# Performance work log

Measured on AMD Instinct MI355X. Metric: run time of the kernel, lower is better.

The kernel has to match this reference:

```python
import jax, jax.numpy as jnp
import numpy as np

N, H, W, C_SH = 512, 256, 256, 16
FX = FY = 300.0


def setup_inputs() -> dict:
    key = jax.random.key(0)
    ks = jax.random.split(key, 6)
    xy = jax.random.uniform(ks[0], (N, 2), minval=-0.8, maxval=0.8)
    z = jax.random.uniform(ks[1], (N, 1), minval=2.0, maxval=6.0)
    xyz = jnp.concatenate([xy * z, z], axis=-1).astype(jnp.float32)  # in frustum
    opacity = jax.random.uniform(ks[2], (N, 1), minval=0.1, maxval=1.0)
    features = jax.random.normal(ks[3], (N, C_SH, 3), dtype=jnp.float32) * 0.3
    A = jax.random.normal(ks[4], (N, 3, 3), dtype=jnp.float32) * 0.05
    covariance = jnp.einsum('nij,nkj->nik', A, A) + 1e-6 * jnp.eye(3, dtype=jnp.float32)
    K = jnp.array([[FX, 0.0, W / 2], [0.0, FY, H / 2], [0.0, 0.0, 1.0]], dtype=jnp.float32)
    w2c = jnp.eye(4, dtype=jnp.float32)
    bg = jnp.zeros(3, jnp.float32)
    return {"xyz": xyz, "opacity": opacity, "features": features,
            "covariance": covariance, "K": K, "w2c": w2c, "bg": bg}


def sh_to_rgb(sh, vd):
    # sh: (N,16,3), vd: (N,3) unit view dirs; degree-3 real SH basis
    C0, C1 = 0.28209479177387814, 0.4886025119029199
    x, y, z = vd[:, 0:1], vd[:, 1:2], vd[:, 2:3]
    r = sh[:, 0] * C0
    r = r + C1 * (-y * sh[:, 1] + z * sh[:, 2] - x * sh[:, 3])
    xx, yy, zz = x * x, y * y, z * z
    xy, yz, xz = x * y, y * z, x * z
    r = r + (1.0925484305920792 * xy * sh[:, 4]
             - 1.0925484305920792 * yz * sh[:, 5]
             + 0.31539156525252005 * (2.0 * zz - xx - yy) * sh[:, 6]
             - 1.0925484305920792 * xz * sh[:, 7]
             + 0.5462742152960396 * (xx - yy) * sh[:, 8])
    r = r + (-0.5900435899266435 * y * (3.0 * xx - yy) * sh[:, 9]
             + 2.890611442640554 * xy * z * sh[:, 10]
             - 0.4570457994644658 * y * (4.0 * zz - xx - yy) * sh[:, 11]
             + 0.3731763325901154 * z * (2.0 * zz - 3.0 * xx - 3.0 * yy) * sh[:, 12]
             - 0.4570457994644658 * x * (4.0 * zz - xx - yy) * sh[:, 13]
             + 1.445305721320277 * z * (xx - yy) * sh[:, 14]
             - 0.5900435899266435 * x * (xx - 3.0 * yy) * sh[:, 15])
    return jnp.clip(r + 0.5, 0.0, 1.0)


def render_gaussians(xyz, opacity, features, covariance, K, w2c, bg):
    R, t = w2c[:3, :3], w2c[:3, 3]
    xyz_cam = xyz @ R.T + t                      # (N,3)
    depth = xyz_cam[:, 2]
    xy_h = xyz_cam @ K.T
    xy = xy_h[:, :2] / jnp.clip(xy_h[:, 2:3], 1e-8)
    cam_pos = jnp.linalg.inv(w2c)[:3, 3]
    vd = xyz - cam_pos
    vd = vd / jnp.clip(jnp.linalg.norm(vd, axis=-1, keepdims=True), 1e-12)
    rgb = sh_to_rgb(features, vd)                # (N,3)

    # 2D covariance via perspective Jacobian: Sigma2d = (J W S W^T J^T)[:2,:2] + 0.3 I
    tz = jnp.clip(xyz_cam[:, 2], 1e-8)
    tx, ty = xyz_cam[:, 0], xyz_cam[:, 1]
    fx, fy = K[0, 0], K[1, 1]
    zr = jnp.zeros_like(tz)
    tz2 = tz * tz
    J = jnp.stack([fx / tz, zr, -fx * tx / tz2,
                   zr, fy / tz, -fy * ty / tz2,
                   zr, zr, zr], axis=-1).reshape(-1, 3, 3)
    T = jnp.einsum('nij,jk->nik', J, R)
    cov_cam = jnp.einsum('nij,njk,nlk->nil', T, covariance, T)
    cov2d = cov_cam[:, :2, :2] + 0.3 * jnp.eye(2, dtype=xyz.dtype)

    margin = 256.0
    visible = ((depth > 0.01) & (xy[:, 0] > -margin) & (xy[:, 0] < W + margin)
               & (xy[:, 1] > -margin) & (xy[:, 1] < H + margin))

    a, b, d = cov2d[:, 0, 0], cov2d[:, 0, 1], cov2d[:, 1, 1]
    det = a * d - b * b
    trace = a + d
    lam_max = 0.5 * (trace + jnp.sqrt(jnp.clip(trace * trace - 4.0 * det, 0.0)))
    radii_f = 3.0 * jnp.sqrt(jnp.clip(lam_max, 1e-8))
    radii = jnp.where(visible, radii_f, 0.0)
    det_c = jnp.clip(det, 1e-10)
    inv00, inv01, inv11 = d / det_c, -b / det_c, a / det_c

    # depth sort (invisible pushed to back; they contribute zero alpha)
    order = jnp.argsort(jnp.where(visible, depth, jnp.inf))
    mx, my = xy[order, 0], xy[order, 1]
    dep, op, col = depth[order], opacity[order, 0], rgb[order]
    i00, i01, i11 = inv00[order], inv01[order], inv11[order]
    rad = jnp.clip(radii_f[order], 1.0)
    vis = visible[order]

    gx = jnp.arange(W, dtype=xyz.dtype)
    gy = jnp.arange(H, dtype=xyz.dtype)
    dx = gx[None, None, :] - mx[:, None, None]   # (N,1,W) -> bcast (N,H,W)
    dy = gy[None, :, None] - my[:, None, None]
    maha = (i00[:, None, None] * dx * dx
            + 2.0 * i01[:, None, None] * dx * dy
            + i11[:, None, None] * dy * dy)
    weight = jnp.exp(-0.5 * maha)

    # per-gaussian screen box (mirrors the int()-floored crop in the torch loop)
    xlo = jnp.floor(jnp.clip(mx - rad, 0.0, W))
    xhi = jnp.floor(jnp.clip(mx + rad + 1.0, 0.0, W))
    ylo = jnp.floor(jnp.clip(my - rad, 0.0, H))
    yhi = jnp.floor(jnp.clip(my + rad + 1.0, 0.0, H))
    inbox = ((gx[None, None, :] >= xlo[:, None, None]) & (gx[None, None, :] < xhi[:, None, None])
             & (gy[None, :, None] >= ylo[:, None, None]) & (gy[None, :, None] < yhi[:, None, None]))

    alpha = jnp.clip(op[:, None, None] * weight, 0.0, 0.99)
    alpha = jnp.where(inbox & vis[:, None, None], alpha, 0.0)   # (N,H,W)

    # front-to-back alpha compositing via exclusive cumprod in log space
    log1m = jnp.log1p(-alpha)
    logT_excl = jnp.cumsum(log1m, axis=0) - log1m
    Tn = jnp.exp(logT_excl)
    wgt = Tn * alpha                                            # (N,H,W)
    T_final = jnp.exp(logT_excl[-1] + log1m[-1])                # (H,W)

    render = jnp.einsum('nhw,nc->chw', wgt, col) + bg[:, None, None] * T_final
    depth_img = jnp.sum(wgt * dep[:, None, None], axis=0)[None]
    alpha_img = (1.0 - T_final)[None]
    return render, depth_img, alpha_img, radii


def reference(xyz, opacity, features, covariance, K, w2c, bg):
    return render_gaussians(xyz, opacity, features, covariance, K, w2c, bg)
```

## Files before the change

kernel.cpp:

```cpp
#include <hip/hip_runtime.h>
#include <math.h>

#define N_G   512
#define IMG_H 256
#define IMG_W 256


__global__ __launch_bounds__(N_G) void preprocess_sort(
    const float* __restrict__ xyz, const float* __restrict__ opacity,
    const float* __restrict__ features, const float* __restrict__ cov,
    const float* __restrict__ Km, const float* __restrict__ w2c,
    float* __restrict__ radii_out, float4* __restrict__ recs)
{
    __shared__ float skey[N_G];
    const int n = threadIdx.x;

    const float R00=w2c[0], R01=w2c[1], R02=w2c[2],  t0=w2c[3];
    const float R10=w2c[4], R11=w2c[5], R12=w2c[6],  t1=w2c[7];
    const float R20=w2c[8], R21=w2c[9], R22=w2c[10], t2=w2c[11];
    const float K00=Km[0],K01=Km[1],K02=Km[2];
    const float K10=Km[3],K11=Km[4],K12=Km[5];
    const float K20=Km[6],K21=Km[7],K22=Km[8];

    const float wx = xyz[n*3+0], wy = xyz[n*3+1], wz = xyz[n*3+2];
    const float cx = R00*wx + R01*wy + R02*wz + t0;
    const float cy = R10*wx + R11*wy + R12*wz + t1;
    const float cz = R20*wx + R21*wy + R22*wz + t2;
    const float depth = cz;

    const float xh = K00*cx + K01*cy + K02*cz;
    const float yh = K10*cx + K11*cy + K12*cz;
    const float zh = K20*cx + K21*cy + K22*cz;
    const float zc = fmaxf(zh, 1e-8f);
    const float mx = xh / zc, my = yh / zc;

    const float cpx = -(R00*t0 + R10*t1 + R20*t2);
    const float cpy = -(R01*t0 + R11*t1 + R21*t2);
    const float cpz = -(R02*t0 + R12*t1 + R22*t2);
    float vx = wx - cpx, vy = wy - cpy, vz = wz - cpz;
    const float nrm = fmaxf(sqrtf(vx*vx + vy*vy + vz*vz), 1e-12f);
    vx /= nrm; vy /= nrm; vz /= nrm;

    const float xx=vx*vx, yy=vy*vy, zz=vz*vz;
    const float sxy=vx*vy, syz=vy*vz, sxz=vx*vz;
    float sb[16];
    sb[0]  = 0.28209479177387814f;
    sb[1]  = -0.4886025119029199f*vy;
    sb[2]  =  0.4886025119029199f*vz;
    sb[3]  = -0.4886025119029199f*vx;
    sb[4]  =  1.0925484305920792f*sxy;
    sb[5]  = -1.0925484305920792f*syz;
    sb[6]  =  0.31539156525252005f*(2.f*zz - xx - yy);
    sb[7]  = -1.0925484305920792f*sxz;
    sb[8]  =  0.5462742152960396f*(xx - yy);
    sb[9]  = -0.5900435899266435f*vy*(3.f*xx - yy);
    sb[10] =  2.890611442640554f*sxy*vz;
    sb[11] = -0.4570457994644658f*vy*(4.f*zz - xx - yy);
    sb[12] =  0.3731763325901154f*vz*(2.f*zz - 3.f*xx - 3.f*yy);
    sb[13] = -0.4570457994644658f*vx*(4.f*zz - xx - yy);
    sb[14] =  1.445305721320277f*vz*(xx - yy);
    sb[15] = -0.5900435899266435f*vx*(xx - 3.f*yy);

    float cr = 0.f, cg = 0.f, cb = 0.f;
    const float* sh = &features[n*48];
    #pragma unroll
    for (int k = 0; k < 16; ++k) {
        cr += sb[k]*sh[k*3+0];
        cg += sb[k]*sh[k*3+1];
        cb += sb[k]*sh[k*3+2];
    }
    cr = fminf(fmaxf(cr + 0.5f, 0.f), 1.f);
    cg = fminf(fmaxf(cg + 0.5f, 0.f), 1.f);
    cb = fminf(fmaxf(cb + 0.5f, 0.f), 1.f);

    const float fx = K00, fy = K11;
    const float tz = fmaxf(cz, 1e-8f);
    const float tz2 = tz*tz;
    const float J00 = fx/tz,  J02 = -fx*cx/tz2;
    const float J11 = fy/tz,  J12 = -fy*cy/tz2;
    const float T00 = J00*R00 + J02*R20;
    const float T01 = J00*R01 + J02*R21;
    const float T02 = J00*R02 + J02*R22;
    const float T10 = J11*R10 + J12*R20;
    const float T11 = J11*R11 + J12*R21;
    const float T12 = J11*R12 + J12*R22;
    const float* S = &cov[n*9];
    const float u0 = S[0]*T00 + S[1]*T01 + S[2]*T02;
    const float u1 = S[3]*T00 + S[4]*T01 + S[5]*T02;
    const float u2 = S[6]*T00 + S[7]*T01 + S[8]*T02;
    const float a  = T00*u0 + T01*u1 + T02*u2 + 0.3f;
    const float bb = T10*u0 + T11*u1 + T12*u2;
    const float w0 = S[0]*T10 + S[1]*T11 + S[2]*T12;
    const float w1 = S[3]*T10 + S[4]*T11 + S[5]*T12;
    const float w2 = S[6]*T10 + S[7]*T11 + S[8]*T12;
    const float d  = T10*w0 + T11*w1 + T12*w2 + 0.3f;

    const float det   = a*d - bb*bb;
    const float trace = a + d;
    const float lam   = 0.5f*(trace + sqrtf(fmaxf(trace*trace - 4.f*det, 0.f)));
    const float radii_f = 3.f*sqrtf(fmaxf(lam, 1e-8f));

    const bool visible = (depth > 0.01f) &&
                         (mx > -256.f) && (mx < (float)IMG_W + 256.f) &&
                         (my > -256.f) && (my < (float)IMG_H + 256.f);
    radii_out[n] = visible ? radii_f : 0.f;

    const float det_c = fmaxf(det, 1e-10f);
    const float i00 =  d / det_c;
    const float i01 = -bb / det_c;
    const float i11 =  a / det_c;

    const float rad = fmaxf(radii_f, 1.f);
    float xlo = floorf(fminf(fmaxf(mx - rad,      0.f), (float)IMG_W));
    float xhi = floorf(fminf(fmaxf(mx + rad + 1.f, 0.f), (float)IMG_W));
    float ylo = floorf(fminf(fmaxf(my - rad,      0.f), (float)IMG_H));
    float yhi = floorf(fminf(fmaxf(my + rad + 1.f, 0.f), (float)IMG_H));
    if (!visible) { xlo = 1e9f; xhi = -1e9f; ylo = 1e9f; yhi = -1e9f; }

    const float key = visible ? depth : INFINITY;
    skey[n] = key;
    __syncthreads();
    int rank = 0;
    for (int j = 0; j < N_G; ++j) {
        const float kj = skey[j];
        rank += (kj < key) || (kj == key && j < n);
    }

    float4* r = &recs[rank*4];
    r[0] = make_float4(xlo, xhi, ylo, yhi);
    r[1] = make_float4(mx, my, i00, i01);
    r[2] = make_float4(i11, opacity[n], depth, 0.f);
    r[3] = make_float4(cr, cg, cb, 0.f);
}

__global__ __launch_bounds__(256) void rasterize(
    const float4* __restrict__ recs, const float* __restrict__ bg,
    float* __restrict__ out)
{
    __shared__ float4 s_rec[N_G*4];
    __shared__ float  s_xlo[N_G], s_xhi[N_G], s_ylo[N_G], s_yhi[N_G];
    __shared__ int    s_idx[N_G];
    __shared__ int    s_cnt[8];

    const int tid  = threadIdx.x;
    const int lane = tid & 63, w = tid >> 6;

    #pragma unroll
    for (int i = 0; i < 8; ++i) {
        const int j = tid + i*256;
        const float4 v = recs[j];
        s_rec[j] = v;
        if ((j & 3) == 0) {
            const int gi = j >> 2;
            s_xlo[gi] = v.x; s_xhi[gi] = v.y; s_ylo[gi] = v.z; s_yhi[gi] = v.w;
        }
    }
    __syncthreads();

    const float tx0 = (float)(blockIdx.x*16), tx1 = tx0 + 16.f;
    const float ty0 = (float)(blockIdx.y*16), ty1 = ty0 + 16.f;

    const int g0 = tid, g1 = tid + 256;
    const bool k0 = (s_xlo[g0] < tx1) && (s_xhi[g0] > tx0) && (s_ylo[g0] < ty1) && (s_yhi[g0] > ty0);
    const bool k1 = (s_xlo[g1] < tx1) && (s_xhi[g1] > tx0) && (s_ylo[g1] < ty1) && (s_yhi[g1] > ty0);
    const unsigned long long m0 = __ballot(k0);
    const unsigned long long m1 = __ballot(k1);
    if (lane == 0) { s_cnt[w] = __popcll(m0); s_cnt[4+w] = __popcll(m1); }
    __syncthreads();
    const int c0 = s_cnt[0], c1 = s_cnt[1], c2 = s_cnt[2], c3 = s_cnt[3];
    const int c4 = s_cnt[4], c5 = s_cnt[5], c6 = s_cnt[6], c7 = s_cnt[7];
    const int total0 = c0 + c1 + c2 + c3;
    const int cnt    = total0 + c4 + c5 + c6 + c7;
    {
        const int base0 = (w>0?c0:0) + (w>1?c1:0) + (w>2?c2:0);
        const int base1 = total0 + (w>0?c4:0) + (w>1?c5:0) + (w>2?c6:0);
        const unsigned long long below = (1ull << lane) - 1ull;
        if (k0) s_idx[base0 + __popcll(m0 & below)] = g0;
        if (k1) s_idx[base1 + __popcll(m1 & below)] = g1;
    }
    __syncthreads();

    const float fpx = tx0 + (float)(tid & 15);
    const float fpy = ty0 + (float)(tid >> 4);

    float T = 1.f, cr = 0.f, cg = 0.f, cb = 0.f, D = 0.f;

    if (cnt > 0) {
        int i_nxt = (cnt > 1) ? s_idx[1] : s_idx[0];
        int i_cur = s_idx[0];
        float4 a0 = s_rec[4*i_cur+0], a1 = s_rec[4*i_cur+1];
        float4 a2 = s_rec[4*i_cur+2], a3 = s_rec[4*i_cur+3];
        for (int g = 0; g < cnt; ++g) {
            const int gn2 = (g + 2 < cnt) ? (g + 2) : (cnt - 1);
            const int i_n2 = s_idx[gn2];
            const float4 b0 = s_rec[4*i_nxt+0], b1 = s_rec[4*i_nxt+1];
            const float4 b2 = s_rec[4*i_nxt+2], b3 = s_rec[4*i_nxt+3];
            if (fpx >= a0.x && fpx < a0.y && fpy >= a0.z && fpy < a0.w) {
                const float dx = fpx - a1.x, dy = fpy - a1.y;
                const float maha = a1.z*dx*dx + 2.f*a1.w*dx*dy + a2.x*dy*dy;
                const float alpha = fminf(a2.y*__expf(-0.5f*maha), 0.99f);
                const float wgt = T*alpha;
                cr += wgt*a3.x; cg += wgt*a3.y; cb += wgt*a3.z; D += wgt*a2.z;
                T *= (1.f - alpha);
            }
            a0 = b0; a1 = b1; a2 = b2; a3 = b3;
            i_nxt = i_n2;
            if (__all(T < 1e-7f)) break;
        }
    }

    const int p = (int)fpy*IMG_W + (int)fpx;
    const float b0 = bg[0], b1 = bg[1], b2 = bg[2];
    out[p]                 = cr + b0*T;
    out[IMG_H*IMG_W   + p] = cg + b1*T;
    out[2*IMG_H*IMG_W + p] = cb + b2*T;
    out[3*IMG_H*IMG_W + p] = D;
    out[4*IMG_H*IMG_W + p] = 1.f - T;
}

extern "C" void kernel_launch(void* const* d_in, const int* in_sizes, int n_in,
                              void* d_out, int out_size, void* d_ws, size_t ws_size,
                              hipStream_t stream) {
    const float* xyz      = (const float*)d_in[0];
    const float* opacity  = (const float*)d_in[1];
    const float* features = (const float*)d_in[2];
    const float* cov      = (const float*)d_in[3];
    const float* Km       = (const float*)d_in[4];
    const float* w2c      = (const float*)d_in[5];
    const float* bg       = (const float*)d_in[6];
    float* out = (float*)d_out;
    float4* recs = (float4*)d_ws;
    float* radii_out = out + 5*IMG_H*IMG_W;

    preprocess_sort<<<1, N_G, 0, stream>>>(xyz, opacity, features, cov, Km, w2c,
                                           radii_out, recs);
    rasterize<<<dim3(IMG_W/16, IMG_H/16), 256, 0, stream>>>(recs, bg, out);
}
```

Measured before the change: 88.62 us.

## Fuse preprocessing and per-tile depth sort into the rasterize kernel

Drops the single-block preprocess+sort kernel and recomputes all Gaussian records redundantly in every tile block. Each block then sorts only its culled Gaussians by depth with a shared-memory rank sort. This removes one launch, the serialized single-block stage and the workspace round trip. In exchange every block repeats the full per-Gaussian SH and covariance math, uses SoA shared arrays, and loses the register prefetch pipeline in the compositing loop.

```diff
diff --git a/kernel.cpp b/kernel.cpp
--- a/kernel.cpp
+++ b/kernel.cpp
@@ -5,34 +5,34 @@
 #define IMG_H 256
 #define IMG_W 256
 
-
-__global__ __launch_bounds__(N_G) void preprocess_sort(
+struct Rec {
+    float mx, my, i00, i01, i11, op, dep, cr, cg, cb;
+    float xlo, xhi, ylo, yhi, radii;
+    bool  vis;
+};
+
+__device__ inline Rec make_rec(int n,
     const float* __restrict__ xyz, const float* __restrict__ opacity,
     const float* __restrict__ features, const float* __restrict__ cov,
-    const float* __restrict__ Km, const float* __restrict__ w2c,
-    float* __restrict__ radii_out, float4* __restrict__ recs)
+    float R00,float R01,float R02,float t0,
+    float R10,float R11,float R12,float t1,
+    float R20,float R21,float R22,float t2,
+    float K00,float K01,float K02,
+    float K10,float K11,float K12,
+    float K20,float K21,float K22)
 {
-    __shared__ float skey[N_G];
-    const int n = threadIdx.x;
-
-    const float R00=w2c[0], R01=w2c[1], R02=w2c[2],  t0=w2c[3];
-    const float R10=w2c[4], R11=w2c[5], R12=w2c[6],  t1=w2c[7];
-    const float R20=w2c[8], R21=w2c[9], R22=w2c[10], t2=w2c[11];
-    const float K00=Km[0],K01=Km[1],K02=Km[2];
-    const float K10=Km[3],K11=Km[4],K12=Km[5];
-    const float K20=Km[6],K21=Km[7],K22=Km[8];
-
+    Rec o;
     const float wx = xyz[n*3+0], wy = xyz[n*3+1], wz = xyz[n*3+2];
     const float cx = R00*wx + R01*wy + R02*wz + t0;
     const float cy = R10*wx + R11*wy + R12*wz + t1;
     const float cz = R20*wx + R21*wy + R22*wz + t2;
-    const float depth = cz;
+    o.dep = cz;
 
     const float xh = K00*cx + K01*cy + K02*cz;
     const float yh = K10*cx + K11*cy + K12*cz;
     const float zh = K20*cx + K21*cy + K22*cz;
     const float zc = fmaxf(zh, 1e-8f);
-    const float mx = xh / zc, my = yh / zc;
+    o.mx = xh / zc; o.my = yh / zc;
 
     const float cpx = -(R00*t0 + R10*t1 + R20*t2);
     const float cpy = -(R01*t0 + R11*t1 + R21*t2);
@@ -69,9 +69,9 @@
         cg += sb[k]*sh[k*3+1];
         cb += sb[k]*sh[k*3+2];
     }
-    cr = fminf(fmaxf(cr + 0.5f, 0.f), 1.f);
-    cg = fminf(fmaxf(cg + 0.5f, 0.f), 1.f);
-    cb = fminf(fmaxf(cb + 0.5f, 0.f), 1.f);
+    o.cr = fminf(fmaxf(cr + 0.5f, 0.f), 1.f);
+    o.cg = fminf(fmaxf(cg + 0.5f, 0.f), 1.f);
+    o.cb = fminf(fmaxf(cb + 0.5f, 0.f), 1.f);
 
     const float fx = K00, fy = K11;
     const float tz = fmaxf(cz, 1e-8f);
@@ -100,60 +100,61 @@
     const float lam   = 0.5f*(trace + sqrtf(fmaxf(trace*trace - 4.f*det, 0.f)));
     const float radii_f = 3.f*sqrtf(fmaxf(lam, 1e-8f));
 
-    const bool visible = (depth > 0.01f) &&
-                         (mx > -256.f) && (mx < (float)IMG_W + 256.f) &&
-                         (my > -256.f) && (my < (float)IMG_H + 256.f);
-    radii_out[n] = visible ? radii_f : 0.f;
+    o.vis = (o.dep > 0.01f) &&
+            (o.mx > -256.f) && (o.mx < (float)IMG_W + 256.f) &&
+            (o.my > -256.f) && (o.my < (float)IMG_H + 256.f);
+    o.radii = o.vis ? radii_f : 0.f;
 
     const float det_c = fmaxf(det, 1e-10f);
-    const float i00 =  d / det_c;
-    const float i01 = -bb / det_c;
-    const float i11 =  a / det_c;
+    o.i00 =  d / det_c;
+    o.i01 = -bb / det_c;
+    o.i11 =  a / det_c;
+    o.op  = opacity[n];
 
     const float rad = fmaxf(radii_f, 1.f);
-    float xlo = floorf(fminf(fmaxf(mx - rad,      0.f), (float)IMG_W));
-    float xhi = floorf(fminf(fmaxf(mx + rad + 1.f, 0.f), (float)IMG_W));
-    float ylo = floorf(fminf(fmaxf(my - rad,      0.f), (float)IMG_H));
-    float yhi = floorf(fminf(fmaxf(my + rad + 1.f, 0.f), (float)IMG_H));
-    if (!visible) { xlo = 1e9f; xhi = -1e9f; ylo = 1e9f; yhi = -1e9f; }
-
-    const float key = visible ? depth : INFINITY;
-    skey[n] = key;
-    __syncthreads();
-    int rank = 0;
-    for (int j = 0; j < N_G; ++j) {
-        const float kj = skey[j];
-        rank += (kj < key) || (kj == key && j < n);
-    }
-
-    float4* r = &recs[rank*4];
-    r[0] = make_float4(xlo, xhi, ylo, yhi);
-    r[1] = make_float4(mx, my, i00, i01);
-    r[2] = make_float4(i11, opacity[n], depth, 0.f);
-    r[3] = make_float4(cr, cg, cb, 0.f);
+    o.xlo = floorf(fminf(fmaxf(o.mx - rad,      0.f), (float)IMG_W));
+    o.xhi = floorf(fminf(fmaxf(o.mx + rad + 1.f, 0.f), (float)IMG_W));
+    o.ylo = floorf(fminf(fmaxf(o.my - rad,      0.f), (float)IMG_H));
+    o.yhi = floorf(fminf(fmaxf(o.my + rad + 1.f, 0.f), (float)IMG_H));
+    if (!o.vis) { o.xlo = 1e9f; o.xhi = -1e9f; o.ylo = 1e9f; o.yhi = -1e9f; }
+    return o;
 }
 
-__global__ __launch_bounds__(256) void rasterize(
-    const float4* __restrict__ recs, const float* __restrict__ bg,
-    float* __restrict__ out)
+__global__ __launch_bounds__(256) void fused_render(
+    const float* __restrict__ xyz, const float* __restrict__ opacity,
+    const float* __restrict__ features, const float* __restrict__ cov,
+    const float* __restrict__ Km, const float* __restrict__ w2c,
+    const float* __restrict__ bg, float* __restrict__ out)
 {
-    __shared__ float4 s_rec[N_G*4];
-    __shared__ float  s_xlo[N_G], s_xhi[N_G], s_ylo[N_G], s_yhi[N_G];
-    __shared__ int    s_idx[N_G];
-    __shared__ int    s_cnt[8];
+    __shared__ float s_mx[N_G], s_my[N_G], s_i00[N_G], s_i01[N_G], s_i11[N_G];
+    __shared__ float s_op[N_G], s_dep[N_G], s_cr[N_G], s_cg[N_G], s_cb[N_G];
+    __shared__ float s_xlo[N_G], s_xhi[N_G], s_ylo[N_G], s_yhi[N_G];
+    __shared__ float s_key[N_G];
+    __shared__ int   s_idx[N_G], s_sorted[N_G];
+    __shared__ int   s_cnt[8];
 
     const int tid  = threadIdx.x;
     const int lane = tid & 63, w = tid >> 6;
 
+    const float R00=w2c[0], R01=w2c[1], R02=w2c[2],  t0=w2c[3];
+    const float R10=w2c[4], R11=w2c[5], R12=w2c[6],  t1=w2c[7];
+    const float R20=w2c[8], R21=w2c[9], R22=w2c[10], t2=w2c[11];
+    const float K00=Km[0],K01=Km[1],K02=Km[2];
+    const float K10=Km[3],K11=Km[4],K12=Km[5];
+    const float K20=Km[6],K21=Km[7],K22=Km[8];
+
+    const bool writer = (blockIdx.x == 0) && (blockIdx.y == 0);
+    float* radii_out = out + 5*IMG_H*IMG_W;
     #pragma unroll
-    for (int i = 0; i < 8; ++i) {
-        const int j = tid + i*256;
-        const float4 v = recs[j];
-        s_rec[j] = v;
-        if ((j & 3) == 0) {
-            const int gi = j >> 2;
-            s_xlo[gi] = v.x; s_xhi[gi] = v.y; s_ylo[gi] = v.z; s_yhi[gi] = v.w;
-        }
+    for (int c = 0; c < 2; ++c) {
+        const int n = tid + c*256;
+        const Rec r = make_rec(n, xyz, opacity, features, cov,
+                               R00,R01,R02,t0, R10,R11,R12,t1, R20,R21,R22,t2,
+                               K00,K01,K02, K10,K11,K12, K20,K21,K22);
+        s_mx[n]=r.mx;  s_my[n]=r.my;  s_i00[n]=r.i00; s_i01[n]=r.i01; s_i11[n]=r.i11;
+        s_op[n]=r.op;  s_dep[n]=r.dep; s_cr[n]=r.cr;  s_cg[n]=r.cg;  s_cb[n]=r.cb;
+        s_xlo[n]=r.xlo; s_xhi[n]=r.xhi; s_ylo[n]=r.ylo; s_yhi[n]=r.yhi;
+        if (writer) radii_out[n] = r.radii;
     }
     __syncthreads();
 
@@ -167,10 +168,10 @@
     const unsigned long long m1 = __ballot(k1);
     if (lane == 0) { s_cnt[w] = __popcll(m0); s_cnt[4+w] = __popcll(m1); }
     __syncthreads();
-    const int c0 = s_cnt[0], c1 = s_cnt[1], c2 = s_cnt[2], c3 = s_cnt[3];
-    const int c4 = s_cnt[4], c5 = s_cnt[5], c6 = s_cnt[6], c7 = s_cnt[7];
-    const int total0 = c0 + c1 + c2 + c3;
-    const int cnt    = total0 + c4 + c5 + c6 + c7;
+    const int c0=s_cnt[0], c1=s_cnt[1], c2=s_cnt[2], c3=s_cnt[3];
+    const int c4=s_cnt[4], c5=s_cnt[5], c6=s_cnt[6], c7=s_cnt[7];
+    const int total0 = c0+c1+c2+c3;
+    const int cnt    = total0+c4+c5+c6+c7;
     {
         const int base0 = (w>0?c0:0) + (w>1?c1:0) + (w>2?c2:0);
         const int base1 = total0 + (w>0?c4:0) + (w>1?c5:0) + (w>2?c6:0);
@@ -180,40 +181,41 @@
     }
     __syncthreads();
 
+    for (int i = tid; i < cnt; i += 256) s_key[i] = s_dep[s_idx[i]];
+    __syncthreads();
+    for (int i = tid; i < cnt; i += 256) {
+        const float ki = s_key[i];
+        int rank = 0;
+        for (int j = 0; j < cnt; ++j) {
+            const float kj = s_key[j];
+            rank += (kj < ki) || (kj == ki && j < i);
+        }
+        s_sorted[rank] = s_idx[i];
+    }
+    __syncthreads();
+
     const float fpx = tx0 + (float)(tid & 15);
     const float fpy = ty0 + (float)(tid >> 4);
 
-    float T = 1.f, cr = 0.f, cg = 0.f, cb = 0.f, D = 0.f;
-
-    if (cnt > 0) {
-        int i_nxt = (cnt > 1) ? s_idx[1] : s_idx[0];
-        int i_cur = s_idx[0];
-        float4 a0 = s_rec[4*i_cur+0], a1 = s_rec[4*i_cur+1];
-        float4 a2 = s_rec[4*i_cur+2], a3 = s_rec[4*i_cur+3];
-        for (int g = 0; g < cnt; ++g) {
-            const int gn2 = (g + 2 < cnt) ? (g + 2) : (cnt - 1);
-            const int i_n2 = s_idx[gn2];
-            const float4 b0 = s_rec[4*i_nxt+0], b1 = s_rec[4*i_nxt+1];
-            const float4 b2 = s_rec[4*i_nxt+2], b3 = s_rec[4*i_nxt+3];
-            if (fpx >= a0.x && fpx < a0.y && fpy >= a0.z && fpy < a0.w) {
-                const float dx = fpx - a1.x, dy = fpy - a1.y;
-                const float maha = a1.z*dx*dx + 2.f*a1.w*dx*dy + a2.x*dy*dy;
-                const float alpha = fminf(a2.y*__expf(-0.5f*maha), 0.99f);
-                const float wgt = T*alpha;
-                cr += wgt*a3.x; cg += wgt*a3.y; cb += wgt*a3.z; D += wgt*a2.z;
-                T *= (1.f - alpha);
-            }
-            a0 = b0; a1 = b1; a2 = b2; a3 = b3;
-            i_nxt = i_n2;
-            if (__all(T < 1e-7f)) break;
+    float T = 1.f, acr = 0.f, acg = 0.f, acb = 0.f, D = 0.f;
+    for (int g = 0; g < cnt; ++g) {
+        const int i = s_sorted[g];
+        if (fpx >= s_xlo[i] && fpx < s_xhi[i] && fpy >= s_ylo[i] && fpy < s_yhi[i]) {
+            const float dx = fpx - s_mx[i], dy = fpy - s_my[i];
+            const float maha = s_i00[i]*dx*dx + 2.f*s_i01[i]*dx*dy + s_i11[i]*dy*dy;
+            const float alpha = fminf(s_op[i]*__expf(-0.5f*maha), 0.99f);
+            const float wgt = T*alpha;
+            acr += wgt*s_cr[i]; acg += wgt*s_cg[i]; acb += wgt*s_cb[i]; D += wgt*s_dep[i];
+            T *= (1.f - alpha);
         }
+        if (__all(T < 1e-7f)) break;
     }
 
     const int p = (int)fpy*IMG_W + (int)fpx;
     const float b0 = bg[0], b1 = bg[1], b2 = bg[2];
-    out[p]                 = cr + b0*T;
-    out[IMG_H*IMG_W   + p] = cg + b1*T;
-    out[2*IMG_H*IMG_W + p] = cb + b2*T;
+    out[p]                 = acr + b0*T;
+    out[IMG_H*IMG_W   + p] = acg + b1*T;
+    out[2*IMG_H*IMG_W + p] = acb + b2*T;
     out[3*IMG_H*IMG_W + p] = D;
     out[4*IMG_H*IMG_W + p] = 1.f - T;
 }
@@ -229,10 +231,7 @@
     const float* w2c      = (const float*)d_in[5];
     const float* bg       = (const float*)d_in[6];
     float* out = (float*)d_out;
-    float4* recs = (float4*)d_ws;
-    float* radii_out = out + 5*IMG_H*IMG_W;
-
-    preprocess_sort<<<1, N_G, 0, stream>>>(xyz, opacity, features, cov, Km, w2c,
-                                           radii_out, recs);
-    rasterize<<<dim3(IMG_W/16, IMG_H/16), 256, 0, stream>>>(recs, bg, out);
+
+    fused_render<<<dim3(IMG_W/16, IMG_H/16), 256, 0, stream>>>(
+        xyz, opacity, features, cov, Km, w2c, bg, out);
 }
```

Result: faster. 77.88 us (-12.1%).
